# Kernel tuning notes

Measured on AMD Instinct MI355X. Metric: run time of the kernel, lower is better.

## Reference

```python
import jax, jax.numpy as jnp
import numpy as np

N = 50000      # nodes
E = 800000     # edges (avg degree 16)
IN = 128       # in_dim == hidden_dim*num_heads so residuals fire
D = 32         # hidden_dim (per-head)
H = 4          # num_heads
OUT = 64       # out_dim (final layer has 1 head)
NEG_SLOPE = 0.2
LN_EPS = 1e-5


def setup_inputs() -> dict:
    key = jax.random.key(0)
    ks = jax.random.split(key, 16)
    rn = lambda k, s: jax.random.normal(k, s, jnp.float32) * 0.05
    return {
        "features": jax.random.normal(ks[0], (N, IN), jnp.float32),
        "edge_weight": jax.random.uniform(ks[1], (E,), jnp.float32),
        "src": jax.random.randint(ks[2], (E,), 0, N),
        "dst": jax.random.randint(ks[3], (E,), 0, N),
        "W0": rn(ks[4], (IN, H * D)), "al0": rn(ks[5], (H, D)), "ar0": rn(ks[6], (H, D)), "lam0": jnp.float32(1.0),
        "W1": rn(ks[7], (H * D, H * D)), "al1": rn(ks[8], (H, D)), "ar1": rn(ks[9], (H, D)), "lam1": jnp.float32(1.0),
        "W2": rn(ks[10], (H * D, OUT)), "al2": rn(ks[11], (1, OUT)), "ar2": rn(ks[12], (1, OUT)), "lam2": jnp.float32(1.0),
        "g0": jnp.ones((H * D,), jnp.float32), "b0": jnp.zeros((H * D,), jnp.float32),
        "g1": jnp.ones((H * D,), jnp.float32), "b1": jnp.zeros((H * D,), jnp.float32),
    }


def _gat_layer(h, W, al, ar, lam, src, dst, ew):
    n = h.shape[0]
    heads, d = al.shape
    ft = (h @ W).reshape(n, heads, d)                      # [N,H,D]
    el = jnp.sum(ft * al[None], axis=-1)                   # [N,H]
    er = jnp.sum(ft * ar[None], axis=-1)                   # [N,H]
    e = el[src] + er[dst] + lam * ew[:, None]              # [E,H] u_add_v + weight bias
    e = jax.nn.leaky_relu(e, NEG_SLOPE)
    # edge softmax over incoming edges of each dst node
    m = jax.ops.segment_max(e, dst, num_segments=n)        # [N,H]
    ex = jnp.exp(e - m[dst])
    s = jax.ops.segment_sum(ex, dst, num_segments=n)       # [N,H]
    a = ex / s[dst]                                        # [E,H]
    # u_mul_e + sum aggregation
    msg = ft[src] * a[:, :, None]                          # [E,H,D]
    return jax.ops.segment_sum(msg, dst, num_segments=n)   # [N,H,D]


def _layer_norm(x, g, b):
    mu = jnp.mean(x, axis=-1, keepdims=True)
    var = jnp.mean((x - mu) ** 2, axis=-1, keepdims=True)
    return (x - mu) * jax.lax.rsqrt(var + LN_EPS) * g + b


def _forward(features, edge_weight, src, dst,
             W0, al0, ar0, lam0, W1, al1, ar1, lam1, W2, al2, ar2, lam2,
             g0, b0, g1, b1):
    n = features.shape[0]
    h = features
    # layer 0
    h1 = _gat_layer(h, W0, al0, ar0, lam0, src, dst, edge_weight)
    h1 = jax.nn.elu(h1).reshape(n, -1)
    h1 = _layer_norm(h1, g0, b0)
    if h1.shape == h.shape:
        h1 = h1 + h
    # layer 1
    h2 = _gat_layer(h1, W1, al1, ar1, lam1, src, dst, edge_weight)
    h2 = jax.nn.elu(h2).reshape(n, -1)
    h2 = _layer_norm(h2, g1, b1)
    h2 = h2 + h1
    # layer 2 (single head, no activation)
    out = _gat_layer(h2, W2, al2, ar2, lam2, src, dst, edge_weight).reshape(n, -1)
    return out


def reference(features, edge_weight, src, dst,
              W0, al0, ar0, lam0, W1, al1, ar1, lam1, W2, al2, ar2, lam2,
              g0, b0, g1, b1):
    # eval mode: dropout off and _add_noise is identity, so noisy == clean
    h_clean = _forward(features, edge_weight, src, dst,
                       W0, al0, ar0, lam0, W1, al1, ar1, lam1, W2, al2, ar2, lam2,
                       g0, b0, g1, b1)
    return (h_clean, h_clean)
```

## Files before the change

### kernel.cpp

```cpp
#include <hip/hip_runtime.h>

#define NEG_SLOPE 0.2f
#define LN_EPS 1e-5f

typedef __attribute__((ext_vector_type(8))) short bf16x8;
typedef __attribute__((ext_vector_type(4))) float f32x4;

__device__ inline unsigned short f2bf(float f) {
    unsigned u = __float_as_uint(f);
    unsigned r = u + 0x7FFFu + ((u >> 16) & 1u);
    return (unsigned short)(r >> 16);
}

__device__ inline void unpack8(uint4 u, float* f) {
    f[0] = __uint_as_float(u.x << 16);
    f[1] = __uint_as_float(u.x & 0xFFFF0000u);
    f[2] = __uint_as_float(u.y << 16);
    f[3] = __uint_as_float(u.y & 0xFFFF0000u);
    f[4] = __uint_as_float(u.z << 16);
    f[5] = __uint_as_float(u.z & 0xFFFF0000u);
    f[6] = __uint_as_float(u.w << 16);
    f[7] = __uint_as_float(u.w & 0xFFFF0000u);
}


__global__ void prep_kernel(const int* __restrict__ dst, int* __restrict__ counts,
                            int* __restrict__ rank, int E, int RB,
                            const float* __restrict__ W0, const float* __restrict__ W1,
                            const float* __restrict__ W2, unsigned short* __restrict__ Wt0,
                            unsigned short* __restrict__ Wt1,
                            unsigned short* __restrict__ Wt2) {
    int bid = blockIdx.x;
    if (bid < RB) {
        int i = bid * 256 + threadIdx.x;
        if (i < E) rank[i] = atomicAdd(&counts[dst[i] * 16], 1);
    } else {
        int row = (bid - RB) * 2 + (threadIdx.x >> 7);
        int k = threadIdx.x & 127;
        if (row < 128) {
            Wt0[row * 128 + k] = f2bf(W0[k * 128 + row]);
        } else if (row < 256) {
            int c = row - 128;
            Wt1[c * 128 + k] = f2bf(W1[k * 128 + c]);
        } else {
            int c = row - 256;
            Wt2[c * 128 + k] = f2bf(W2[k * 64 + c]);
        }
    }
}

__global__ __launch_bounds__(256) void scan1_kernel(const int* __restrict__ counts,
                                                    int* __restrict__ bsum, int n) {
    __shared__ int lds[256];
    int t = threadIdx.x;
    int i = blockIdx.x * 256 + t;
    lds[t] = (i < n) ? counts[i * 16] : 0;
    __syncthreads();
    for (int off = 128; off > 0; off >>= 1) {
        int v = (t < off) ? lds[t + off] : 0;
        __syncthreads();
        if (t < off) lds[t] += v;
        __syncthreads();
    }
    if (t == 0) bsum[blockIdx.x] = lds[0];
}

__global__ __launch_bounds__(256) void scan3_kernel(const int* __restrict__ counts,
                                                    const int* __restrict__ bsum,
                                                    int* __restrict__ rowptr, int n, int E,
                                                    int nscan) {
    __shared__ int lds[256];
    int t = threadIdx.x;
    lds[t] = (t < nscan) ? bsum[t] : 0;
    __syncthreads();
    for (int off = 1; off < 256; off <<= 1) {
        int v = (t >= off) ? lds[t - off] : 0;
        __syncthreads();
        lds[t] += v;
        __syncthreads();
    }
    int boff = (blockIdx.x > 0) ? lds[blockIdx.x - 1] : 0;
    __syncthreads();
    int i = blockIdx.x * 256 + t;
    int c = (i < n) ? counts[i * 16] : 0;
    lds[t] = c;
    __syncthreads();
    for (int off = 1; off < 256; off <<= 1) {
        int v = (t >= off) ? lds[t - off] : 0;
        __syncthreads();
        lds[t] += v;
        __syncthreads();
    }
    if (i < n) rowptr[i] = boff + lds[t] - c;
    if (i == n) rowptr[n] = E;
}

__global__ void place_kernel(const int* __restrict__ src, const int* __restrict__ dst,
                             const float* __restrict__ ew, const int* __restrict__ rowptr,
                             const int* __restrict__ rank, unsigned* __restrict__ edge_p,
                             int E) {
    int i = blockIdx.x * blockDim.x + threadIdx.x;
    if (i < E) {
        int p = rowptr[dst[i]] + rank[i];
        edge_p[p] = ((unsigned)f2bf(ew[i]) << 16) | (unsigned)src[i];
    }
}


template <int NT, int H, bool A32>
__global__ __launch_bounds__(256) void gemm_mfma(const void* __restrict__ Ap,
                                                 const unsigned short* __restrict__ Wt,
                                                 const float* __restrict__ al,
                                                 const float* __restrict__ ar,
                                                 unsigned short* __restrict__ ftb,
                                                 float* __restrict__ el,
                                                 float* __restrict__ er, int n) {
    constexpr int LDA = 136;
    constexpr int D = NT * 16 / H;
    __shared__ unsigned short As[64 * LDA];
    __shared__ unsigned short Ws[NT * 16 * LDA];
    int t = threadIdx.x;
    int row0 = blockIdx.x * 64;

    if constexpr (A32) {
        const float4* A4 = (const float4*)Ap;
        #pragma unroll
        for (int j = 0; j < 8; ++j) {
            int idx = t + j * 256;
            int r = idx >> 5;
            int c4 = idx & 31;
            int row = row0 + r;
            float4 v = (row < n) ? A4[(size_t)row * 32 + c4] : make_float4(0.f, 0.f, 0.f, 0.f);
            unsigned p0 = (unsigned)f2bf(v.x) | ((unsigned)f2bf(v.y) << 16);
            unsigned p1 = (unsigned)f2bf(v.z) | ((unsigned)f2bf(v.w) << 16);
            *(uint2*)&As[r * LDA + c4 * 4] = make_uint2(p0, p1);
        }
    } else {
        const uint4* A16 = (const uint4*)Ap;
        #pragma unroll
        for (int j = 0; j < 4; ++j) {
            int idx = t + j * 256;
            int r = idx >> 4;
            int c8 = idx & 15;
            int row = row0 + r;
            uint4 v = (row < n) ? A16[(size_t)row * 16 + c8] : make_uint4(0, 0, 0, 0);
            *(uint4*)&As[r * LDA + c8 * 8] = v;
        }
    }
    const uint4* Wg = (const uint4*)Wt;
    #pragma unroll
    for (int j = 0; j < NT; ++j) {
        int idx = t + j * 256;
        int r = idx >> 4;
        int c8 = idx & 15;
        *(uint4*)&Ws[r * LDA + c8 * 8] = Wg[idx];
    }
    __syncthreads();

    int w = t >> 6, lane = t & 63;
    int m = lane & 15, q = lane >> 4;
    f32x4 acc[NT] = {};
    const unsigned short* ap = &As[(w * 16 + m) * LDA + q * 8];
    #pragma unroll
    for (int kk = 0; kk < 4; ++kk) {
        bf16x8 a = *(const bf16x8*)(ap + kk * 32);
        #pragma unroll
        for (int nt = 0; nt < NT; ++nt) {
            bf16x8 b = *(const bf16x8*)&Ws[(nt * 16 + m) * LDA + kk * 32 + q * 8];
            acc[nt] = __builtin_amdgcn_mfma_f32_16x16x32_bf16(a, b, acc[nt], 0, 0, 0);
        }
    }

    float alv[NT], arv[NT];
    #pragma unroll
    for (int nt = 0; nt < NT; ++nt) {
        alv[nt] = al[nt * 16 + m];
        arv[nt] = ar[nt * 16 + m];
    }

    int orow = row0 + w * 16 + q * 4;
    #pragma unroll
    for (int r = 0; r < 4; ++r) {
        int row = orow + r;
        float pl[H] = {}, pr[H] = {};
        #pragma unroll
        for (int nt = 0; nt < NT; ++nt) {
            int h = (nt * 16) / D;
            pl[h] = fmaf(acc[nt][r], alv[nt], pl[h]);
            pr[h] = fmaf(acc[nt][r], arv[nt], pr[h]);
        }
        #pragma unroll
        for (int off = 1; off < 16; off <<= 1) {
            #pragma unroll
            for (int h = 0; h < H; ++h) {
                pl[h] += __shfl_xor(pl[h], off, 64);
                pr[h] += __shfl_xor(pr[h], off, 64);
            }
        }
        if (row < n) {
            #pragma unroll
            for (int nt = 0; nt < NT; ++nt)
                ftb[(size_t)row * (NT * 16) + nt * 16 + m] = f2bf(acc[nt][r]);
            if (m < H) {
                float vl = pl[0], vr = pr[0];
                #pragma unroll
                for (int h = 1; h < H; ++h)
                    if (m == h) { vl = pl[h]; vr = pr[h]; }
                el[row * H + m] = vl;
                er[row * H + m] = vr;
            }
        }
    }
}


__device__ inline void accum8(float* ax, uint4 u, float p) {
    ax[0] = fmaf(p, __uint_as_float(u.x << 16), ax[0]);
    ax[1] = fmaf(p, __uint_as_float(u.x & 0xFFFF0000u), ax[1]);
    ax[2] = fmaf(p, __uint_as_float(u.y << 16), ax[2]);
    ax[3] = fmaf(p, __uint_as_float(u.y & 0xFFFF0000u), ax[3]);
    ax[4] = fmaf(p, __uint_as_float(u.z << 16), ax[4]);
    ax[5] = fmaf(p, __uint_as_float(u.z & 0xFFFF0000u), ax[5]);
    ax[6] = fmaf(p, __uint_as_float(u.w << 16), ax[6]);
    ax[7] = fmaf(p, __uint_as_float(u.w & 0xFFFF0000u), ax[7]);
}

template <bool PREV32>
__global__ __launch_bounds__(256) void gat_agg_ln(
    const int* __restrict__ rowptr, const unsigned* __restrict__ edge_p,
    const uint4* __restrict__ ftb4, const float* __restrict__ el,
    const float* __restrict__ er, const float* __restrict__ lam_p,
    const float* __restrict__ g, const float* __restrict__ b,
    const void* __restrict__ prevp, uint4* __restrict__ outb, int n) {
    int node = blockIdx.x * 16 + (threadIdx.x >> 4);
    if (node >= n) return;
    int li = threadIdx.x & 15;
    int head = li >> 2;
    float lam = lam_p[0];
    float erv = er[node * 4 + head];
    int s0 = rowptr[node], s1 = rowptr[node + 1];
    float ax[8] = {};
    float s = 0.f;

    int i = s0;
    for (; i + 4 <= s1; i += 4) {
        unsigned e0 = edge_p[i], e1 = edge_p[i + 1], e2 = edge_p[i + 2], e3 = edge_p[i + 3];
        unsigned sn0 = e0 & 0xFFFFu, sn1 = e1 & 0xFFFFu, sn2 = e2 & 0xFFFFu, sn3 = e3 & 0xFFFFu;
        uint4 u0 = ftb4[(size_t)sn0 * 16 + li];
        uint4 u1 = ftb4[(size_t)sn1 * 16 + li];
        uint4 u2 = ftb4[(size_t)sn2 * 16 + li];
        uint4 u3 = ftb4[(size_t)sn3 * 16 + li];
        float l0 = el[sn0 * 4 + head];
        float l1 = el[sn1 * 4 + head];
        float l2 = el[sn2 * 4 + head];
        float l3 = el[sn3 * 4 + head];
        float v0 = l0 + erv + lam * __uint_as_float(e0 & 0xFFFF0000u);
        float v1 = l1 + erv + lam * __uint_as_float(e1 & 0xFFFF0000u);
        float v2 = l2 + erv + lam * __uint_as_float(e2 & 0xFFFF0000u);
        float v3 = l3 + erv + lam * __uint_as_float(e3 & 0xFFFF0000u);
        v0 = fmaxf(v0, NEG_SLOPE * v0);
        v1 = fmaxf(v1, NEG_SLOPE * v1);
        v2 = fmaxf(v2, NEG_SLOPE * v2);
        v3 = fmaxf(v3, NEG_SLOPE * v3);
        float p0 = __expf(v0), p1 = __expf(v1), p2 = __expf(v2), p3 = __expf(v3);
        accum8(ax, u0, p0);
        accum8(ax, u1, p1);
        accum8(ax, u2, p2);
        accum8(ax, u3, p3);
        s += (p0 + p1) + (p2 + p3);
    }
    for (; i < s1; ++i) {
        unsigned e = edge_p[i];
        unsigned sn = e & 0xFFFFu;
        uint4 u = ftb4[(size_t)sn * 16 + li];
        float v = el[sn * 4 + head] + erv + lam * __uint_as_float(e & 0xFFFF0000u);
        v = fmaxf(v, NEG_SLOPE * v);
        float p = __expf(v);
        accum8(ax, u, p);
        s += p;
    }

    float inv = (s > 0.f) ? 1.f / s : 0.f;
    float x[8];
    float sum = 0.f, sq = 0.f;
    #pragma unroll
    for (int d = 0; d < 8; ++d) {
        float v = ax[d] * inv;
        v = (v > 0.f) ? v : expm1f(v);
        x[d] = v;
        sum += v;
        sq += v * v;
    }
    #pragma unroll
    for (int off = 1; off < 16; off <<= 1) {
        sum += __shfl_xor(sum, off, 16);
        sq += __shfl_xor(sq, off, 16);
    }
    float mu = sum * (1.f / 128.f);
    float var = sq * (1.f / 128.f) - mu * mu;
    float rs = rsqrtf(var + LN_EPS);

    const float4* g4 = (const float4*)g;
    const float4* b4 = (const float4*)b;
    float pv[8];
    if constexpr (PREV32) {
        const float4* p4 = (const float4*)prevp;
        #pragma unroll
        for (int h = 0; h < 2; ++h) {
            float4 v = p4[(size_t)node * 32 + li * 2 + h];
            pv[h * 4 + 0] = v.x; pv[h * 4 + 1] = v.y;
            pv[h * 4 + 2] = v.z; pv[h * 4 + 3] = v.w;
        }
    } else {
        unpack8(((const uint4*)prevp)[(size_t)node * 16 + li], pv);
    }
    float y[8];
    #pragma unroll
    for (int h = 0; h < 2; ++h) {
        float4 gv = g4[li * 2 + h];
        float4 bv = b4[li * 2 + h];
        y[h * 4 + 0] = (x[h * 4 + 0] - mu) * rs * gv.x + bv.x + pv[h * 4 + 0];
        y[h * 4 + 1] = (x[h * 4 + 1] - mu) * rs * gv.y + bv.y + pv[h * 4 + 1];
        y[h * 4 + 2] = (x[h * 4 + 2] - mu) * rs * gv.z + bv.z + pv[h * 4 + 2];
        y[h * 4 + 3] = (x[h * 4 + 3] - mu) * rs * gv.w + bv.w + pv[h * 4 + 3];
    }
    uint4 o;
    o.x = (unsigned)f2bf(y[0]) | ((unsigned)f2bf(y[1]) << 16);
    o.y = (unsigned)f2bf(y[2]) | ((unsigned)f2bf(y[3]) << 16);
    o.z = (unsigned)f2bf(y[4]) | ((unsigned)f2bf(y[5]) << 16);
    o.w = (unsigned)f2bf(y[6]) | ((unsigned)f2bf(y[7]) << 16);
    outb[(size_t)node * 16 + li] = o;
}

__global__ __launch_bounds__(256) void gat_agg_out(
    const int* __restrict__ rowptr, const unsigned* __restrict__ edge_p,
    const uint2* __restrict__ ftb2, const float* __restrict__ el,
    const float* __restrict__ er, const float* __restrict__ lam_p,
    float* __restrict__ out, int n) {
    int node = blockIdx.x * 16 + (threadIdx.x >> 4);
    if (node >= n) return;
    int li = threadIdx.x & 15;
    float lam = lam_p[0];
    float erv = er[node];
    int s0 = rowptr[node], s1 = rowptr[node + 1];
    float ax[4] = {};
    float s = 0.f;

    int i = s0;
    for (; i + 4 <= s1; i += 4) {
        unsigned e0 = edge_p[i], e1 = edge_p[i + 1], e2 = edge_p[i + 2], e3 = edge_p[i + 3];
        unsigned sn0 = e0 & 0xFFFFu, sn1 = e1 & 0xFFFFu, sn2 = e2 & 0xFFFFu, sn3 = e3 & 0xFFFFu;
        uint2 u0 = ftb2[(size_t)sn0 * 16 + li];
        uint2 u1 = ftb2[(size_t)sn1 * 16 + li];
        uint2 u2 = ftb2[(size_t)sn2 * 16 + li];
        uint2 u3 = ftb2[(size_t)sn3 * 16 + li];
        float l0 = el[sn0], l1 = el[sn1], l2 = el[sn2], l3 = el[sn3];
        float v0 = l0 + erv + lam * __uint_as_float(e0 & 0xFFFF0000u);
        float v1 = l1 + erv + lam * __uint_as_float(e1 & 0xFFFF0000u);
        float v2 = l2 + erv + lam * __uint_as_float(e2 & 0xFFFF0000u);
        float v3 = l3 + erv + lam * __uint_as_float(e3 & 0xFFFF0000u);
        v0 = fmaxf(v0, NEG_SLOPE * v0);
        v1 = fmaxf(v1, NEG_SLOPE * v1);
        v2 = fmaxf(v2, NEG_SLOPE * v2);
        v3 = fmaxf(v3, NEG_SLOPE * v3);
        float p0 = __expf(v0), p1 = __expf(v1), p2 = __expf(v2), p3 = __expf(v3);
        ax[0] = fmaf(p0, __uint_as_float(u0.x << 16), ax[0]);
        ax[1] = fmaf(p0, __uint_as_float(u0.x & 0xFFFF0000u), ax[1]);
        ax[2] = fmaf(p0, __uint_as_float(u0.y << 16), ax[2]);
        ax[3] = fmaf(p0, __uint_as_float(u0.y & 0xFFFF0000u), ax[3]);
        ax[0] = fmaf(p1, __uint_as_float(u1.x << 16), ax[0]);
        ax[1] = fmaf(p1, __uint_as_float(u1.x & 0xFFFF0000u), ax[1]);
        ax[2] = fmaf(p1, __uint_as_float(u1.y << 16), ax[2]);
        ax[3] = fmaf(p1, __uint_as_float(u1.y & 0xFFFF0000u), ax[3]);
        ax[0] = fmaf(p2, __uint_as_float(u2.x << 16), ax[0]);
        ax[1] = fmaf(p2, __uint_as_float(u2.x & 0xFFFF0000u), ax[1]);
        ax[2] = fmaf(p2, __uint_as_float(u2.y << 16), ax[2]);
        ax[3] = fmaf(p2, __uint_as_float(u2.y & 0xFFFF0000u), ax[3]);
        ax[0] = fmaf(p3, __uint_as_float(u3.x << 16), ax[0]);
        ax[1] = fmaf(p3, __uint_as_float(u3.x & 0xFFFF0000u), ax[1]);
        ax[2] = fmaf(p3, __uint_as_float(u3.y << 16), ax[2]);
        ax[3] = fmaf(p3, __uint_as_float(u3.y & 0xFFFF0000u), ax[3]);
        s += (p0 + p1) + (p2 + p3);
    }
    for (; i < s1; ++i) {
        unsigned e = edge_p[i];
        unsigned sn = e & 0xFFFFu;
        uint2 u = ftb2[(size_t)sn * 16 + li];
        float v = el[sn] + erv + lam * __uint_as_float(e & 0xFFFF0000u);
        v = fmaxf(v, NEG_SLOPE * v);
        float p = __expf(v);
        ax[0] = fmaf(p, __uint_as_float(u.x << 16), ax[0]);
        ax[1] = fmaf(p, __uint_as_float(u.x & 0xFFFF0000u), ax[1]);
        ax[2] = fmaf(p, __uint_as_float(u.y << 16), ax[2]);
        ax[3] = fmaf(p, __uint_as_float(u.y & 0xFFFF0000u), ax[3]);
        s += p;
    }

    float inv = (s > 0.f) ? 1.f / s : 0.f;
    float4 y;
    y.x = ax[0] * inv;
    y.y = ax[1] * inv;
    y.z = ax[2] * inv;
    y.w = ax[3] * inv;
    ((float4*)out)[(size_t)node * 16 + li] = y;
    ((float4*)out)[(size_t)(n + node) * 16 + li] = y;
}


extern "C" void kernel_launch(void* const* d_in, const int* in_sizes, int n_in,
                              void* d_out, int out_size, void* d_ws, size_t ws_size,
                              hipStream_t stream) {
    const float* features = (const float*)d_in[0];
    const float* edge_weight = (const float*)d_in[1];
    const int* src = (const int*)d_in[2];
    const int* dst = (const int*)d_in[3];
    const float* W0 = (const float*)d_in[4];
    const float* al0 = (const float*)d_in[5];
    const float* ar0 = (const float*)d_in[6];
    const float* lam0 = (const float*)d_in[7];
    const float* W1 = (const float*)d_in[8];
    const float* al1 = (const float*)d_in[9];
    const float* ar1 = (const float*)d_in[10];
    const float* lam1 = (const float*)d_in[11];
    const float* W2 = (const float*)d_in[12];
    const float* al2 = (const float*)d_in[13];
    const float* ar2 = (const float*)d_in[14];
    const float* lam2 = (const float*)d_in[15];
    const float* g0 = (const float*)d_in[16];
    const float* b0 = (const float*)d_in[17];
    const float* g1 = (const float*)d_in[18];
    const float* b1 = (const float*)d_in[19];

    const int N = in_sizes[0] / 128;
    const int E = in_sizes[1];

    char* w = (char*)d_ws;
    size_t o = 0;
    auto carve = [&](size_t bytes) {
        char* p = w + o;
        o += (bytes + 255) & ~(size_t)255;
        return p;
    };
    int* counts = (int*)carve((size_t)N * 64);
    int* rowptr = (int*)carve((size_t)(N + 1) * 4);
    int* bsum = (int*)carve(256 * 4);
    int* rank = (int*)carve((size_t)E * 4);
    unsigned* edge_p = (unsigned*)carve((size_t)E * 4);
    unsigned short* ftb = (unsigned short*)carve((size_t)N * 128 * 2);
    unsigned short* h1 = (unsigned short*)carve((size_t)N * 128 * 2);
    unsigned short* h2 = (unsigned short*)carve((size_t)N * 128 * 2);
    float* el = (float*)carve((size_t)N * 4 * 4);
    float* er = (float*)carve((size_t)N * 4 * 4);
    unsigned short* Wt0 = (unsigned short*)carve(128 * 128 * 2);
    unsigned short* Wt1 = (unsigned short*)carve(128 * 128 * 2);
    unsigned short* Wt2 = (unsigned short*)carve(64 * 128 * 2);

    const int nscan = (N + 255) / 256;
    const int ngemm = (N + 63) / 64;
    const int nagg = (N + 15) / 16;
    const int RB = (E + 255) / 256;

    hipMemsetAsync(counts, 0, (size_t)N * 64, stream);
    prep_kernel<<<RB + 160, 256, 0, stream>>>(dst, counts, rank, E, RB,
                                              W0, W1, W2, Wt0, Wt1, Wt2);
    scan1_kernel<<<nscan, 256, 0, stream>>>(counts, bsum, N);
    scan3_kernel<<<(N + 1 + 255) / 256, 256, 0, stream>>>(counts, bsum, rowptr, N, E, nscan);
    place_kernel<<<(E + 255) / 256, 256, 0, stream>>>(src, dst, edge_weight, rowptr,
                                                      rank, edge_p, E);

    gemm_mfma<8, 4, true><<<ngemm, 256, 0, stream>>>(features, Wt0, al0, ar0,
                                                     ftb, el, er, N);
    gat_agg_ln<true><<<nagg, 256, 0, stream>>>(rowptr, edge_p, (const uint4*)ftb, el, er,
                                               lam0, g0, b0, features, (uint4*)h1, N);
    gemm_mfma<8, 4, false><<<ngemm, 256, 0, stream>>>(h1, Wt1, al1, ar1, ftb, el, er, N);
    gat_agg_ln<false><<<nagg, 256, 0, stream>>>(rowptr, edge_p, (const uint4*)ftb, el, er,
                                                lam1, g1, b1, h1, (uint4*)h2, N);
    gemm_mfma<4, 1, false><<<ngemm, 256, 0, stream>>>(h2, Wt2, al2, ar2, ftb, el, er, N);
    gat_agg_out<<<nagg, 256, 0, stream>>>(rowptr, edge_p, (const uint2*)ftb,
                                          el, er, lam2, (float*)d_out, N);
}
```

Before: 295.3 us.

## Fuse CSR build into cooperative kernel and degree-sort nodes for aggregation

Replaces the memset plus four CSR-construction kernels with one cooperative kernel that uses grid-wide syncs between counting, scanning and placement, cutting launch overhead. It also builds a degree histogram and a node permutation sorted by in-degree, so that the aggregation kernels process nodes of similar degree within each wavefront and waste fewer lanes on load imbalance. The cost is grid syncs inside a fixed 1024-block cooperative launch, plus an extra indirection through the permutation, which scatters output writes and node-indexed loads.

New measurement: 960.3 us. 3.25x slower.

```diff
diff --git a/kernel.cpp b/kernel.cpp
--- a/kernel.cpp
+++ b/kernel.cpp
@@ -1,7 +1,12 @@
 #include <hip/hip_runtime.h>
+#include <hip/hip_cooperative_groups.h>
+
+namespace cg = cooperative_groups;
 
 #define NEG_SLOPE 0.2f
 #define LN_EPS 1e-5f
+#define DMAX 128
+#define CGRID 1024
 
 typedef __attribute__((ext_vector_type(8))) short bf16x8;
 typedef __attribute__((ext_vector_type(4))) float f32x4;
@@ -24,85 +29,124 @@
 }
 
 
-__global__ void prep_kernel(const int* __restrict__ dst, int* __restrict__ counts,
-                            int* __restrict__ rank, int E, int RB,
-                            const float* __restrict__ W0, const float* __restrict__ W1,
-                            const float* __restrict__ W2, unsigned short* __restrict__ Wt0,
-                            unsigned short* __restrict__ Wt1,
-                            unsigned short* __restrict__ Wt2) {
-    int bid = blockIdx.x;
-    if (bid < RB) {
-        int i = bid * 256 + threadIdx.x;
-        if (i < E) rank[i] = atomicAdd(&counts[dst[i] * 16], 1);
-    } else {
-        int row = (bid - RB) * 2 + (threadIdx.x >> 7);
-        int k = threadIdx.x & 127;
-        if (row < 128) {
-            Wt0[row * 128 + k] = f2bf(W0[k * 128 + row]);
-        } else if (row < 256) {
-            int c = row - 128;
-            Wt1[c * 128 + k] = f2bf(W1[k * 128 + c]);
-        } else {
-            int c = row - 256;
-            Wt2[c * 128 + k] = f2bf(W2[k * 64 + c]);
-        }
-    }
-}
-
-__global__ __launch_bounds__(256) void scan1_kernel(const int* __restrict__ counts,
-                                                    int* __restrict__ bsum, int n) {
-    __shared__ int lds[256];
-    int t = threadIdx.x;
-    int i = blockIdx.x * 256 + t;
-    lds[t] = (i < n) ? counts[i * 16] : 0;
-    __syncthreads();
-    for (int off = 128; off > 0; off >>= 1) {
-        int v = (t < off) ? lds[t + off] : 0;
-        __syncthreads();
-        if (t < off) lds[t] += v;
-        __syncthreads();
-    }
-    if (t == 0) bsum[blockIdx.x] = lds[0];
-}
-
-__global__ __launch_bounds__(256) void scan3_kernel(const int* __restrict__ counts,
-                                                    const int* __restrict__ bsum,
-                                                    int* __restrict__ rowptr, int n, int E,
-                                                    int nscan) {
-    __shared__ int lds[256];
-    int t = threadIdx.x;
-    lds[t] = (t < nscan) ? bsum[t] : 0;
-    __syncthreads();
-    for (int off = 1; off < 256; off <<= 1) {
-        int v = (t >= off) ? lds[t - off] : 0;
-        __syncthreads();
-        lds[t] += v;
-        __syncthreads();
-    }
-    int boff = (blockIdx.x > 0) ? lds[blockIdx.x - 1] : 0;
-    __syncthreads();
-    int i = blockIdx.x * 256 + t;
-    int c = (i < n) ? counts[i * 16] : 0;
-    lds[t] = c;
-    __syncthreads();
-    for (int off = 1; off < 256; off <<= 1) {
-        int v = (t >= off) ? lds[t - off] : 0;
-        __syncthreads();
-        lds[t] += v;
-        __syncthreads();
-    }
-    if (i < n) rowptr[i] = boff + lds[t] - c;
-    if (i == n) rowptr[n] = E;
-}
-
-__global__ void place_kernel(const int* __restrict__ src, const int* __restrict__ dst,
-                             const float* __restrict__ ew, const int* __restrict__ rowptr,
-                             const int* __restrict__ rank, unsigned* __restrict__ edge_p,
-                             int E) {
-    int i = blockIdx.x * blockDim.x + threadIdx.x;
-    if (i < E) {
+__global__ __launch_bounds__(256) void csr_coop(
+    const int* __restrict__ src, const int* __restrict__ dst,
+    const float* __restrict__ ew, int* __restrict__ counts, int* __restrict__ rank,
+    int* __restrict__ bsum, int* __restrict__ rowptr, unsigned* __restrict__ edge_p,
+    int* __restrict__ deghist, int* __restrict__ dcur, int* __restrict__ perm,
+    int n, int E,
+    const float* __restrict__ W0, const float* __restrict__ W1,
+    const float* __restrict__ W2, unsigned short* __restrict__ Wt0,
+    unsigned short* __restrict__ Wt1, unsigned short* __restrict__ Wt2) {
+    cg::grid_group grid = cg::this_grid();
+    __shared__ int sb[1280];
+    const int T = gridDim.x * 256;
+    const int gtid = blockIdx.x * 256 + threadIdx.x;
+    const int t = threadIdx.x;
+
+    for (int i = gtid; i < n * 16; i += T) counts[i] = 0;
+    for (int i = gtid; i < (DMAX + 1) * 16; i += T) { deghist[i] = 0; dcur[i] = 0; }
+    for (int i = gtid; i < 320 * 128; i += T) {
+        int row = i >> 7, k = i & 127;
+        if (row < 128) Wt0[row * 128 + k] = f2bf(W0[k * 128 + row]);
+        else if (row < 256) Wt1[(row - 128) * 128 + k] = f2bf(W1[k * 128 + (row - 128)]);
+        else Wt2[(row - 256) * 128 + k] = f2bf(W2[k * 64 + (row - 256)]);
+    }
+    grid.sync();
+
+    for (int i = gtid; i < E; i += T) rank[i] = atomicAdd(&counts[dst[i] * 16], 1);
+    grid.sync();
+
+    const int CH = (n + gridDim.x - 1) / gridDim.x;
+    {
+        int i = blockIdx.x * CH + t;
+        int c = (t < CH && i < n) ? counts[i * 16] : 0;
+        sb[t] = c;
+        __syncthreads();
+        for (int off = 128; off > 0; off >>= 1) {
+            int v = (t < off) ? sb[t + off] : 0;
+            __syncthreads();
+            if (t < off) sb[t] += v;
+            __syncthreads();
+        }
+        if (t == 0) bsum[blockIdx.x] = sb[0];
+    }
+    grid.sync();
+
+    {
+        int* elems = sb;
+        int* ps = sb + 1024;
+        int l[4];
+        int lsum = 0;
+        #pragma unroll
+        for (int k = 0; k < 4; ++k) {
+            int idx = t * 4 + k;
+            l[k] = (idx < (int)gridDim.x) ? bsum[idx] : 0;
+            lsum += l[k];
+        }
+        ps[t] = lsum;
+        __syncthreads();
+        for (int off = 1; off < 256; off <<= 1) {
+            int v = (t >= off) ? ps[t - off] : 0;
+            __syncthreads();
+            ps[t] += v;
+            __syncthreads();
+        }
+        int ebase = ps[t] - lsum;
+        elems[t * 4 + 0] = ebase;
+        elems[t * 4 + 1] = ebase + l[0];
+        elems[t * 4 + 2] = ebase + l[0] + l[1];
+        elems[t * 4 + 3] = ebase + l[0] + l[1] + l[2];
+        __syncthreads();
+        int boff = elems[blockIdx.x];
+        __syncthreads();
+        int i = blockIdx.x * CH + t;
+        int c = (t < CH && i < n) ? counts[i * 16] : 0;
+        sb[t] = c;
+        __syncthreads();
+        for (int off = 1; off < 256; off <<= 1) {
+            int v = (t >= off) ? sb[t - off] : 0;
+            __syncthreads();
+            sb[t] += v;
+            __syncthreads();
+        }
+        if (t < CH && i < n) rowptr[i] = boff + sb[t] - c;
+        if (i == n) rowptr[n] = E;
+    }
+    grid.sync();
+
+    for (int i = gtid; i < E; i += T) {
         int p = rowptr[dst[i]] + rank[i];
         edge_p[p] = ((unsigned)f2bf(ew[i]) << 16) | (unsigned)src[i];
+    }
+    for (int i = gtid; i < n; i += T) {
+        int d = counts[i * 16];
+        d = (d > DMAX) ? DMAX : d;
+        atomicAdd(&deghist[d * 16], 1);
+    }
+    grid.sync();
+
+    {
+        int v = (t <= DMAX) ? deghist[t * 16] : 0;
+        __syncthreads();
+        sb[t] = v;
+        __syncthreads();
+        for (int off = 1; off < 256; off <<= 1) {
+            int x = (t >= off) ? sb[t - off] : 0;
+            __syncthreads();
+            sb[t] += x;
+            __syncthreads();
+        }
+        int excl = sb[t] - v;
+        __syncthreads();
+        sb[t] = excl;
+        __syncthreads();
+        for (int i = gtid; i < n; i += T) {
+            int d = counts[i * 16];
+            d = (d > DMAX) ? DMAX : d;
+            int pos = sb[d] + atomicAdd(&dcur[d * 16], 1);
+            perm[pos] = i;
+        }
     }
 }
 
@@ -227,13 +271,15 @@
 
 template <bool PREV32>
 __global__ __launch_bounds__(256) void gat_agg_ln(
-    const int* __restrict__ rowptr, const unsigned* __restrict__ edge_p,
-    const uint4* __restrict__ ftb4, const float* __restrict__ el,
-    const float* __restrict__ er, const float* __restrict__ lam_p,
-    const float* __restrict__ g, const float* __restrict__ b,
-    const void* __restrict__ prevp, uint4* __restrict__ outb, int n) {
-    int node = blockIdx.x * 16 + (threadIdx.x >> 4);
-    if (node >= n) return;
+    const int* __restrict__ perm, const int* __restrict__ rowptr,
+    const unsigned* __restrict__ edge_p, const uint4* __restrict__ ftb4,
+    const float* __restrict__ el, const float* __restrict__ er,
+    const float* __restrict__ lam_p, const float* __restrict__ g,
+    const float* __restrict__ b, const void* __restrict__ prevp,
+    uint4* __restrict__ outb, int n) {
+    int gidx = blockIdx.x * 16 + (threadIdx.x >> 4);
+    if (gidx >= n) return;
+    int node = perm[gidx];
     int li = threadIdx.x & 15;
     int head = li >> 2;
     float lam = lam_p[0];
@@ -333,12 +379,13 @@
 }
 
 __global__ __launch_bounds__(256) void gat_agg_out(
-    const int* __restrict__ rowptr, const unsigned* __restrict__ edge_p,
-    const uint2* __restrict__ ftb2, const float* __restrict__ el,
-    const float* __restrict__ er, const float* __restrict__ lam_p,
-    float* __restrict__ out, int n) {
-    int node = blockIdx.x * 16 + (threadIdx.x >> 4);
-    if (node >= n) return;
+    const int* __restrict__ perm, const int* __restrict__ rowptr,
+    const unsigned* __restrict__ edge_p, const uint2* __restrict__ ftb2,
+    const float* __restrict__ el, const float* __restrict__ er,
+    const float* __restrict__ lam_p, float* __restrict__ out, int n) {
+    int gidx = blockIdx.x * 16 + (threadIdx.x >> 4);
+    if (gidx >= n) return;
+    int node = perm[gidx];
     int li = threadIdx.x & 15;
     float lam = lam_p[0];
     float erv = er[node];
@@ -431,8 +478,8 @@
     const float* g1 = (const float*)d_in[18];
     const float* b1 = (const float*)d_in[19];
 
-    const int N = in_sizes[0] / 128;
-    const int E = in_sizes[1];
+    int N = in_sizes[0] / 128;
+    int E = in_sizes[1];
 
     char* w = (char*)d_ws;
     size_t o = 0;
@@ -443,9 +490,12 @@
     };
     int* counts = (int*)carve((size_t)N * 64);
     int* rowptr = (int*)carve((size_t)(N + 1) * 4);
-    int* bsum = (int*)carve(256 * 4);
+    int* bsum = (int*)carve(CGRID * 4);
     int* rank = (int*)carve((size_t)E * 4);
     unsigned* edge_p = (unsigned*)carve((size_t)E * 4);
+    int* deghist = (int*)carve((DMAX + 1) * 64);
+    int* dcur = (int*)carve((DMAX + 1) * 64);
+    int* perm = (int*)carve((size_t)N * 4);
     unsigned short* ftb = (unsigned short*)carve((size_t)N * 128 * 2);
     unsigned short* h1 = (unsigned short*)carve((size_t)N * 128 * 2);
     unsigned short* h2 = (unsigned short*)carve((size_t)N * 128 * 2);
@@ -455,27 +505,25 @@
     unsigned short* Wt1 = (unsigned short*)carve(128 * 128 * 2);
     unsigned short* Wt2 = (unsigned short*)carve(64 * 128 * 2);
 
-    const int nscan = (N + 255) / 256;
     const int ngemm = (N + 63) / 64;
     const int nagg = (N + 15) / 16;
-    const int RB = (E + 255) / 256;
-
-    hipMemsetAsync(counts, 0, (size_t)N * 64, stream);
-    prep_kernel<<<RB + 160, 256, 0, stream>>>(dst, counts, rank, E, RB,
-                                              W0, W1, W2, Wt0, Wt1, Wt2);
-    scan1_kernel<<<nscan, 256, 0, stream>>>(counts, bsum, N);
-    scan3_kernel<<<(N + 1 + 255) / 256, 256, 0, stream>>>(counts, bsum, rowptr, N, E, nscan);
-    place_kernel<<<(E + 255) / 256, 256, 0, stream>>>(src, dst, edge_weight, rowptr,
-                                                      rank, edge_p, E);
+
+    void* args[] = {(void*)&src, (void*)&dst, (void*)&edge_weight, (void*)&counts,
+                    (void*)&rank, (void*)&bsum, (void*)&rowptr, (void*)&edge_p,
+                    (void*)&deghist, (void*)&dcur, (void*)&perm, (void*)&N, (void*)&E,
+                    (void*)&W0, (void*)&W1, (void*)&W2, (void*)&Wt0, (void*)&Wt1,
+                    (void*)&Wt2};
+    hipLaunchCooperativeKernel((void*)csr_coop, dim3(CGRID), dim3(256), args, 0, stream);
 
     gemm_mfma<8, 4, true><<<ngemm, 256, 0, stream>>>(features, Wt0, al0, ar0,
                                                      ftb, el, er, N);
-    gat_agg_ln<true><<<nagg, 256, 0, stream>>>(rowptr, edge_p, (const uint4*)ftb, el, er,
-                                               lam0, g0, b0, features, (uint4*)h1, N);
+    gat_agg_ln<true><<<nagg, 256, 0, stream>>>(perm, rowptr, edge_p, (const uint4*)ftb,
+                                               el, er, lam0, g0, b0, features,
+                                               (uint4*)h1, N);
     gemm_mfma<8, 4, false><<<ngemm, 256, 0, stream>>>(h1, Wt1, al1, ar1, ftb, el, er, N);
-    gat_agg_ln<false><<<nagg, 256, 0, stream>>>(rowptr, edge_p, (const uint4*)ftb, el, er,
-                                                lam1, g1, b1, h1, (uint4*)h2, N);
+    gat_agg_ln<false><<<nagg, 256, 0, stream>>>(perm, rowptr, edge_p, (const uint4*)ftb,
+                                                el, er, lam1, g1, b1, h1, (uint4*)h2, N);
     gemm_mfma<4, 1, false><<<ngemm, 256, 0, stream>>>(h2, Wt2, al2, ar2, ftb, el, er, N);
-    gat_agg_out<<<nagg, 256, 0, stream>>>(rowptr, edge_p, (const uint2*)ftb,
+    gat_agg_out<<<nagg, 256, 0, stream>>>(perm, rowptr, edge_p, (const uint2*)ftb,
                                           el, er, lam2, (float*)d_out, N);
 }
```
